# Kernel tuning notes

Measured on AMD Instinct MI355X. Metric: run time of the kernel, lower is better.

The kernel has to match this reference:

```python
import jax, jax.numpy as jnp
import numpy as np

T, N, D_OBS = 32, 32, 64
HID, HEADS, MEM, N_ACT = 512, 4, 128, 16
SECTIONS = [HEADS * HID, HEADS, HID, 1, HID, HID, HEADS, 1, 1, 3 * HEADS]
XI = sum(SECTIONS)


def setup_inputs() -> dict:
    key = jax.random.key(0)
    ks = jax.random.split(key, 8)
    s = 0.02
    return {
        "inputs": jax.random.normal(ks[0], (T, N, D_OBS), jnp.float32),
        "w_ih": jax.random.normal(ks[1], (3 * HID, D_OBS), jnp.float32) * s,
        "w_hh": jax.random.normal(ks[2], (3 * HID, HID), jnp.float32) * s,
        "b_ih": jnp.zeros((3 * HID,), jnp.float32),
        "b_hh": jnp.zeros((3 * HID,), jnp.float32),
        "Wf": jax.random.normal(ks[3], (XI, HID), jnp.float32) * s,
        "bf": jnp.zeros((XI,), jnp.float32),
        "Wa": jax.random.normal(ks[4], (N_ACT, HID), jnp.float32) * s,
        "ba": jnp.zeros((N_ACT,), jnp.float32),
        "Wc": jax.random.normal(ks[5], (1, HID), jnp.float32) * s,
        "bc": jnp.zeros((1,), jnp.float32),
    }


def reference(inputs, w_ih, w_hh, b_ih, b_hh, Wf, bf, Wa, ba, Wc, bc):
    idx = np.cumsum(SECTIONS)[:-1]
    eps = 1e-8

    def step(carry, x_t):
        h, wr, u, ww, M, p, L = carry
        # --- GRU cell (torch convention) ---
        gi = x_t @ w_ih.T + b_ih
        gh = h @ w_hh.T + b_hh
        ir, iz, inn = jnp.split(gi, 3, axis=-1)
        hr, hz, hn = jnp.split(gh, 3, axis=-1)
        rg = jax.nn.sigmoid(ir + hr)
        zg = jax.nn.sigmoid(iz + hz)
        ng = jnp.tanh(inn + rg * hn)
        h = (1 - zg) * ng + zg * h
        # --- interface vector xi ---
        xi = jax.nn.relu(h) @ Wf.T + bf
        Kr, Br, kw, bw, e, v, F_hat, ga, gw, Pi = jnp.split(xi, idx, axis=-1)
        Kr = Kr.reshape(N, HEADS, HID)
        Br = jax.nn.softplus(Br)                      # [N,H]
        bw = jax.nn.softplus(bw)                      # [N,1]
        e = jax.nn.sigmoid(e)                         # [N,HID] erase
        v_w = v                                       # [N,HID] write vec
        F_hat = jax.nn.sigmoid(F_hat)                 # [N,H] free gates
        ga = jax.nn.sigmoid(ga)                       # [N,1]
        gw = jax.nn.sigmoid(gw)                       # [N,1]
        Pi = jax.nn.softmax(Pi.reshape(N, HEADS, 3), axis=-1)
        # --- memory retention & usage ---
        psi = jnp.prod(1 - F_hat[..., None] * wr, axis=1)          # [N,MEM]
        u = (u + ww - u * ww) * psi
        # --- allocation weighting via usage sort ---
        phi = jnp.argsort(u, axis=-1)
        u_sorted = jnp.take_along_axis(u, phi, axis=-1)
        excl = jnp.concatenate(
            [jnp.ones((N, 1), u.dtype), jnp.cumprod(u_sorted[:, :-1], axis=-1)], axis=-1)
        a_sorted = (1 - u_sorted) * excl
        alloc = jnp.zeros_like(u).at[jnp.arange(N)[:, None], phi].set(a_sorted)
        # --- content-based write weighting ---
        Mn = jnp.sqrt(jnp.sum(M * M, axis=-1))                     # [N,MEM]
        kwn = jnp.sqrt(jnp.sum(kw * kw, axis=-1, keepdims=True))   # [N,1]
        cos_w = jnp.einsum('nmd,nd->nm', M, kw) / (Mn * kwn + eps)
        cw = jax.nn.softmax(bw * cos_w, axis=-1)
        ww = gw * (ga * alloc + (1 - ga) * cw)                     # [N,MEM]
        # --- memory write (erase + add outer products) ---
        M = M * (1 - ww[..., None] * e[:, None, :]) + ww[..., None] * v_w[:, None, :]
        # --- precedence & temporal link matrix ---
        p = (1 - jnp.sum(ww, axis=-1, keepdims=True)) * p + ww
        L = (1 - ww[..., None] - ww[:, None, :]) * L + ww[..., None] * p[:, None, :]
        # --- forward/backward read weights ---
        fwd_w = jnp.einsum('nij,nhj->nhi', L, wr)
        bwd_w = jnp.einsum('nji,nhj->nhi', L, wr)
        # --- content-based read weighting ---
        Mn2 = jnp.sqrt(jnp.sum(M * M, axis=-1))                    # [N,MEM]
        Krn = jnp.sqrt(jnp.sum(Kr * Kr, axis=-1, keepdims=True))   # [N,H,1]
        cos_r = jnp.einsum('nmd,nhd->nhm', M, Kr) / (Mn2[:, None, :] * Krn + eps)
        cr = jax.nn.softmax(Br[..., None] * cos_r, axis=-1)
        wr = Pi[..., 0:1] * bwd_w + Pi[..., 1:2] * cr + Pi[..., 2:3] * fwd_w
        # --- read vectors, actor, critic ---
        r_read = jnp.einsum('nmd,nhm->nd', M, wr)                  # sum over heads -> [N,HID]
        a_probs = jax.nn.softmax(r_read @ Wa.T + ba, axis=-1)      # [N,N_ACT]
        val = h @ Wc.T + bc                                        # [N,1]
        return (h, wr, u, ww, M, p, L), jnp.concatenate([a_probs, val], axis=-1)

    z = jnp.zeros
    carry0 = (z((N, HID)), z((N, HEADS, MEM)), z((N, MEM)), z((N, MEM)),
              z((N, MEM, HID)), z((N, MEM)), z((N, MEM, MEM)))
    _, outs = jax.lax.scan(step, carry0, inputs)
    return outs  # [T, N, N_ACT+1]
```

## Files before the change

### kernel.cpp

```cpp
#include <hip/hip_runtime.h>
#include <math.h>

#define TT 32
#define NB 32
#define DOBS 64
#define HID 512
#define HEADS 4
#define MEM 128
#define NACT 16
#define XID 3607
#define G3 1536

__device__ __forceinline__ float sigm(float x){ return 1.0f/(1.0f+__expf(-x)); }
__device__ __forceinline__ float splus(float x){ return fmaxf(x,0.f) + log1pf(__expf(-fabsf(x))); }

__device__ __forceinline__ float wsum64(float s){
    s += __shfl_xor(s,1); s += __shfl_xor(s,2); s += __shfl_xor(s,4);
    s += __shfl_xor(s,8); s += __shfl_xor(s,16);
    float t = s;
    asm volatile("v_permlane32_swap_b32 %0, %1" : "+v"(s), "+v"(t));
    return s + t;
}
__device__ __forceinline__ float rsum_hi(float v){
    float t = v;
    asm volatile("v_permlane16_swap_b32 %0, %1" : "+v"(v), "+v"(t));
    v += t;
    float t2 = v;
    asm volatile("v_permlane32_swap_b32 %0, %1" : "+v"(v), "+v"(t2));
    return v + t2;
}

__global__ __launch_bounds__(256) void k_transpose(const float* __restrict__ src,
                                                   float* __restrict__ dst, int R, int C)
{
    __shared__ float tile[32][33];
    int r0 = blockIdx.x*32, c0 = blockIdx.y*32;
    int tx = threadIdx.x, ty = threadIdx.y;
    #pragma unroll
    for (int yy = 0; yy < 32; yy += 8) {
        int r = r0 + ty + yy, c = c0 + tx;
        if (r < R && c < C) tile[ty+yy][tx] = src[(size_t)r*C + c];
    }
    __syncthreads();
    #pragma unroll
    for (int yy = 0; yy < 32; yy += 8) {
        int c = c0 + ty + yy, r = r0 + tx;
        if (r < R && c < C) dst[(size_t)c*R + r] = tile[tx][ty+yy];
    }
}

__global__ __launch_bounds__(384) void k_gru(
    const float* __restrict__ x,
    const float* __restrict__ wihT,
    const float* __restrict__ whhT,
    const float* __restrict__ b_ih,
    const float* __restrict__ b_hh,
    float* __restrict__ h_all,
    float* hG,
    int* flags)
{
    const int n   = blockIdx.x & 31;
    const int s   = blockIdx.x >> 5;
    const int tid = threadIdx.x;
    const int kq  = tid / 96;
    const int c   = tid % 96;
    const int g   = c >> 5;
    const int r0  = g*512 + s*128 + (c & 31)*4;

    __shared__ float hS[512];
    __shared__ float xS[64];
    __shared__ float4 pI[4][96];
    __shared__ float4 pH[4][96];
    __shared__ float grS[128], gzS[128], giN[128], ghN[128];

    for (int i = tid; i < 512; i += 384) hS[i] = 0.f;

    for (int t = 0; t < TT; ++t) {
        if (tid < 64) xS[tid] = x[((size_t)t*NB + n)*DOBS + tid];
        __syncthreads();
        {
            float4 aI = make_float4(0.f,0.f,0.f,0.f);
            float4 aH = make_float4(0.f,0.f,0.f,0.f);
            const int kx0 = kq*16;
            #pragma unroll 4
            for (int k = kx0; k < kx0+16; ++k) {
                float xv = xS[k];
                float4 w = *(const float4*)(wihT + (size_t)k*G3 + r0);
                aI.x += w.x*xv; aI.y += w.y*xv; aI.z += w.z*xv; aI.w += w.w*xv;
            }
            const int kh0 = kq*128;
            #pragma unroll 4
            for (int k = kh0; k < kh0+128; ++k) {
                float hv = hS[k];
                float4 w = *(const float4*)(whhT + (size_t)k*G3 + r0);
                aH.x += w.x*hv; aH.y += w.y*hv; aH.z += w.z*hv; aH.w += w.w*hv;
            }
            pI[kq][c] = aI; pH[kq][c] = aH;
        }
        __syncthreads();
        {
            const int g2 = tid >> 7, d = tid & 127;
            const int c2 = g2*32 + (d>>2), e = d & 3;
            float AI = 0.f, AH = 0.f;
            #pragma unroll
            for (int q = 0; q < 4; ++q) {
                float4 vi = pI[q][c2], vh = pH[q][c2];
                AI += (e==0)?vi.x:(e==1)?vi.y:(e==2)?vi.z:vi.w;
                AH += (e==0)?vh.x:(e==1)?vh.y:(e==2)?vh.z:vh.w;
            }
            const int rg = g2*512 + s*128 + d;
            AI += b_ih[rg]; AH += b_hh[rg];
            if (g2 == 0)      grS[d] = AI + AH;
            else if (g2 == 1) gzS[d] = AI + AH;
            else              { giN[d] = AI; ghN[d] = AH; }
        }
        __syncthreads();
        if (tid < 128) {
            const int D = s*128 + tid;
            float rg = sigm(grS[tid]);
            float zg = sigm(gzS[tid]);
            float ng = tanhf(giN[tid] + rg*ghN[tid]);
            float hn = (1.f-zg)*ng + zg*hS[D];
            h_all[((size_t)t*NB + n)*HID + D] = hn;
            __hip_atomic_store(&hG[n*HID + D], hn, __ATOMIC_RELAXED, __HIP_MEMORY_SCOPE_AGENT);
        }
        __syncthreads();
        if (t+1 < TT) {
            if (tid == 0) {
                __hip_atomic_fetch_add(&flags[n], 1, __ATOMIC_RELEASE, __HIP_MEMORY_SCOPE_AGENT);
                while (__hip_atomic_load(&flags[n], __ATOMIC_ACQUIRE, __HIP_MEMORY_SCOPE_AGENT) < 4*(t+1)) {
                    __builtin_amdgcn_s_sleep(4);
                }
            }
            __syncthreads();
            for (int i = tid; i < 512; i += 384)
                hS[i] = __hip_atomic_load(&hG[n*HID + i], __ATOMIC_RELAXED, __HIP_MEMORY_SCOPE_AGENT);
        }
    }
}

__global__ __launch_bounds__(256) void k_xi(
    const float* __restrict__ h_all,
    const float* __restrict__ Wf,
    const float* __restrict__ bf,
    float* __restrict__ xi_all)
{
    __shared__ float As[16][132];
    __shared__ float Bs[16][68];
    const int jt = blockIdx.x * 64;
    const int it = blockIdx.y * 128;
    const int tid = threadIdx.x;
    const int lc = tid & 15, lr = tid >> 4;
    const int tx = tid & 15, ty = tid >> 4;
    float acc[8][4] = {};

    for (int k0 = 0; k0 < HID; k0 += 16) {
        #pragma unroll
        for (int s = 0; s < 8; ++s) {
            int i = lr*8 + s;
            As[lc][i] = fmaxf(h_all[(size_t)(it + i)*HID + k0 + lc], 0.f);
        }
        #pragma unroll
        for (int s = 0; s < 4; ++s) {
            int j = lr*4 + s;
            Bs[lc][j] = (jt + j < XID) ? Wf[(size_t)(jt + j)*HID + k0 + lc] : 0.f;
        }
        __syncthreads();
        #pragma unroll
        for (int k = 0; k < 16; ++k) {
            float4 a0 = *(const float4*)&As[k][ty*8];
            float4 a1 = *(const float4*)&As[k][ty*8+4];
            float4 bv = *(const float4*)&Bs[k][tx*4];
            float a[8] = {a0.x,a0.y,a0.z,a0.w,a1.x,a1.y,a1.z,a1.w};
            float b[4] = {bv.x,bv.y,bv.z,bv.w};
            #pragma unroll
            for (int u = 0; u < 8; ++u)
                #pragma unroll
                for (int v = 0; v < 4; ++v) acc[u][v] += a[u]*b[v];
        }
        __syncthreads();
    }
    #pragma unroll
    for (int u = 0; u < 8; ++u)
        #pragma unroll
        for (int v = 0; v < 4; ++v) {
            int i = it + ty*8 + u, j = jt + tx*4 + v;
            if (j < XID) xi_all[(size_t)i*XID + j] = acc[u][v] + bf[j];
        }
}

__global__ __launch_bounds__(64) void k_val(
    const float* __restrict__ h_all, const float* __restrict__ Wc,
    const float* __restrict__ bc, float* __restrict__ out)
{
    const int row = blockIdx.x;
    const int lane = threadIdx.x;
    float acc = 0.f;
    for (int d = lane; d < HID; d += 64) acc += h_all[(size_t)row*HID + d]*Wc[d];
    for (int off = 32; off; off >>= 1) acc += __shfl_down(acc, off);
    if (lane == 0) out[(size_t)row*17 + 16] = acc + bc[0];
}

#define LPAD 132
#define SROW2 576
#define DYN_FLOATS (128*LPAD + 16*SROW2)
#define CIDX(d) ((((d)>>6)*68) + ((d)&63))
#define CIDX2(d) ((((d)>>5)*36) + ((d)&31))

__global__ __launch_bounds__(1024) void k_mem(
    const float* __restrict__ xi_all,
    const float* __restrict__ Wa,
    const float* __restrict__ ba,
    float* __restrict__ out)
{
    extern __shared__ __align__(16) float dynS[];
    float* Lm  = dynS;
    float* scr = dynS + 128*LPAD;

    const int n = blockIdx.x;
    const int tid = threadIdx.x;
    const int lane = tid & 63;
    const int wv = tid >> 6;
    const int m8 = tid >> 3;
    const int q8 = tid & 7;
    const int rp = tid >> 4;
    const int ch = tid & 15;
    const int r0 = rp*2, r1 = r0+1;

    __shared__ __align__(16) float KrC[4*576];
    __shared__ __align__(16) float kwC[576], eC[576], vC[576];
    __shared__ __align__(16) float wrC[4*136];
    __shared__ __align__(16) float r_S[512];
    __shared__ float dotK_S[4][132], fwd_S[4][132], bwd_S[4][132];
    __shared__ float u_S[128], ww_S[128], p_S[128], aS_S[128];
    __shared__ float Mn2_S[128], dw_S[128];
    __shared__ float wred[16][6];
    __shared__ float scal_S[8];
    __shared__ float PiRaw[12];
    __shared__ float Pi_S[4][3], Br_S[4], KrN_S[4], F_S[4];
    __shared__ float ba_S[16], logit_S[16];

    float4 Mreg[16];
    #pragma unroll
    for (int i = 0; i < 16; ++i) Mreg[i] = make_float4(0.f,0.f,0.f,0.f);

    for (int i = tid; i < 128*LPAD; i += 1024) Lm[i] = 0.f;
    if (tid < 16) ba_S[tid] = ba[tid];
    if (tid < 128) { u_S[tid]=0.f; ww_S[tid]=0.f; p_S[tid]=0.f; Mn2_S[tid]=0.f; }
    if (tid < 512) wrC[(tid>>7)*136 + CIDX(tid&127)] = 0.f;

    float waR[8];
    #pragma unroll
    for (int j = 0; j < 8; ++j) waR[j] = Wa[(wv<<9) + lane + (j<<6)];

    const bool hasEx = (tid >= 1000 && tid < 1023);
    int exIdx = 0;
    if (tid >= 1000 && tid < 1004)      exIdx = 2048 + (tid - 1000);
    else if (tid == 1004)               exIdx = 2564;
    else if (tid >= 1005 && tid < 1023) exIdx = 3589 + (tid - 1005);

    const float* xi0 = xi_all + (size_t)n*XID;
    float pKrA = xi0[tid];
    float pKrB = xi0[1024 + tid];
    float pkw = 0.f, pv = 0.f, pe = 0.f;
    if (tid < 512) { pkw = xi0[2052 + tid]; pv = xi0[3077 + tid]; }
    else           { pe  = xi0[2565 + (tid - 512)]; }
    float pex = hasEx ? xi0[exIdx] : 0.f;
    __syncthreads();

    for (int t = 0; t < TT; ++t) {
        float ev2 = 0.f, evA = 0.f;

        {
            int d = tid & 511, hh = tid >> 9;
            int co = CIDX2(d);
            KrC[hh*576 + co]     = pKrA;
            KrC[(2+hh)*576 + co] = pKrB;
        }
        if (tid < 512) { int co = CIDX2(tid); kwC[co] = pkw; vC[co] = pv; }
        else { int s2 = tid - 512; eC[CIDX2(s2)] = sigm(pe); }
        if (hasEx) {
            if (tid < 1004)      Br_S[tid-1000] = splus(pex);
            else if (tid==1004)  scal_S[0] = splus(pex);
            else if (tid < 1009) F_S[tid-1005] = sigm(pex);
            else if (tid==1009)  scal_S[1] = sigm(pex);
            else if (tid==1010)  scal_S[2] = sigm(pex);
            else                 PiRaw[tid-1011] = pex;
        }
        {
            float sA = wsum64(pKrA*pKrA);
            float sB = wsum64(pKrB*pKrB);
            float sK = wsum64(pkw*pkw);
            if (lane == 0) { wred[wv][0]=sA; wred[wv][1]=sB; wred[wv][2]=sK; }
        }
        {
            int tn = (t+1 < TT) ? (t+1) : t;
            const float* xin = xi_all + (size_t)(tn*NB + n)*XID;
            pKrA = xin[tid]; pKrB = xin[1024 + tid];
            if (tid < 512) { pkw = xin[2052 + tid]; pv = xin[3077 + tid]; }
            else           { pe  = xin[2565 + (tid - 512)]; }
            if (hasEx) pex = xin[exIdx];
        }
        __syncthreads();

        if (tid < 4) {
            float s = 0.f;
            #pragma unroll
            for (int w = 0; w < 8; ++w) s += wred[(tid&1)*8 + w][tid>>1];
            KrN_S[tid] = sqrtf(s);
        } else if (tid == 4) {
            float s = 0.f;
            #pragma unroll
            for (int w = 0; w < 8; ++w) s += wred[w][2];
            scal_S[3] = sqrtf(s);
        }
        if (tid < 128) {
            int co = CIDX(tid);
            float psi = (1.f - F_S[0]*wrC[co])      * (1.f - F_S[1]*wrC[136+co])
                      * (1.f - F_S[2]*wrC[272+co])  * (1.f - F_S[3]*wrC[408+co]);
            float uu = u_S[tid], w = ww_S[tid];
            u_S[tid] = (uu + w - uu*w)*psi;
        }
        {
            const float* kwp = kwC + ch*36;
            float dw0 = 0.f, dw1 = 0.f;
            #pragma unroll
            for (int c = 0; c < 8; ++c) {
                float4 kk = *(const float4*)(kwp + 4*c);
                float4 x0 = Mreg[c], x1 = Mreg[8+c];
                dw0 += x0.x*kk.x + x0.y*kk.y + x0.z*kk.z + x0.w*kk.w;
                dw1 += x1.x*kk.x + x1.y*kk.y + x1.z*kk.z + x1.w*kk.w;
            }
            dw0 += __shfl_xor(dw0,1); dw0 += __shfl_xor(dw0,2); dw0 += __shfl_xor(dw0,4); dw0 += __shfl_xor(dw0,8);
            dw1 += __shfl_xor(dw1,1); dw1 += __shfl_xor(dw1,2); dw1 += __shfl_xor(dw1,4); dw1 += __shfl_xor(dw1,8);
            if (ch == 0) { dw_S[r0] = dw0; dw_S[r1] = dw1; }
        }
        __syncthreads();

        {
            float um = u_S[m8];
            float pr = 1.f;
            #pragma unroll
            for (int jj = 0; jj < 16; ++jj) {
                int j = jj*8 + q8;
                float uj = u_S[j];
                pr *= ((uj < um) || (uj == um && j < m8)) ? uj : 1.f;
            }
            pr *= __shfl_xor(pr, 1);
            pr *= __shfl_xor(pr, 2);
            pr *= __shfl_xor(pr, 4);
            if (q8 == 0) aS_S[m8] = (1.f - um)*pr;
        }
        if (tid < 128) {
            float cwv = scal_S[0]*dw_S[tid]/(Mn2_S[tid]*scal_S[3] + 1e-8f);
            evA = __expf(cwv);
            float s = wsum64(evA);
            if (lane == 0) wred[wv][1] = s;
        } else if (tid >= 136 && tid < 140) {
            int h = tid - 136;
            float p0 = PiRaw[3*h], p1 = PiRaw[3*h+1], p2 = PiRaw[3*h+2];
            float mx = fmaxf(p0, fmaxf(p1, p2));
            float e0=__expf(p0-mx), e1=__expf(p1-mx), e2=__expf(p2-mx);
            float s = e0+e1+e2;
            Pi_S[h][0]=e0/s; Pi_S[h][1]=e1/s; Pi_S[h][2]=e2/s;
        }
        __syncthreads();

        if (tid < 128) {
            float cwsum = wred[0][1] + wred[1][1];
            float alloc = aS_S[tid];
            float ga = scal_S[1], gw = scal_S[2];
            float w = gw*(ga*alloc + (1.f-ga)*evA/cwsum);
            ww_S[tid] = w;
            float s = wsum64(w);
            if (lane == 0) wred[wv][0] = s;
        }
        __syncthreads();

        if (tid < 128) {
            float sww = wred[0][0] + wred[1][0];
            p_S[tid] = (1.f - sww)*p_S[tid] + ww_S[tid];
        }
        {
            const int base = ch*36;
            const float* ep  = eC + base;
            const float* vp  = vC + base;
            const float* k0p = KrC + base;
            const float* k1p = KrC + 576 + base;
            const float* k2p = KrC + 1152 + base;
            const float* k3p = KrC + 1728 + base;
            const float ww0 = ww_S[r0], ww1 = ww_S[r1];
            float nrm0=0.f, nrm1=0.f;
            float a0=0.f,a1=0.f,a2=0.f,a3=0.f;
            float b0=0.f,b1=0.f,b2=0.f,b3=0.f;
            #pragma unroll
            for (int c = 0; c < 8; ++c) {
                float4 ee = *(const float4*)(ep + 4*c);
                float4 vv = *(const float4*)(vp + 4*c);
                float4 x  = Mreg[c];
                x.x = x.x*(1.f - ww0*ee.x) + ww0*vv.x;
                x.y = x.y*(1.f - ww0*ee.y) + ww0*vv.y;
                x.z = x.z*(1.f - ww0*ee.z) + ww0*vv.z;
                x.w = x.w*(1.f - ww0*ee.w) + ww0*vv.w;
                Mreg[c] = x;
                nrm0 += x.x*x.x + x.y*x.y + x.z*x.z + x.w*x.w;
                float4 y  = Mreg[8+c];
                y.x = y.x*(1.f - ww1*ee.x) + ww1*vv.x;
                y.y = y.y*(1.f - ww1*ee.y) + ww1*vv.y;
                y.z = y.z*(1.f - ww1*ee.z) + ww1*vv.z;
                y.w = y.w*(1.f - ww1*ee.w) + ww1*vv.w;
                Mreg[8+c] = y;
                nrm1 += y.x*y.x + y.y*y.y + y.z*y.z + y.w*y.w;
                float4 k0 = *(const float4*)(k0p + 4*c);
                float4 k1 = *(const float4*)(k1p + 4*c);
                float4 k2 = *(const float4*)(k2p + 4*c);
                float4 k3 = *(const float4*)(k3p + 4*c);
                a0 += x.x*k0.x + x.y*k0.y + x.z*k0.z + x.w*k0.w;
                a1 += x.x*k1.x + x.y*k1.y + x.z*k1.z + x.w*k1.w;
                a2 += x.x*k2.x + x.y*k2.y + x.z*k2.z + x.w*k2.w;
                a3 += x.x*k3.x + x.y*k3.y + x.z*k3.z + x.w*k3.w;
                b0 += y.x*k0.x + y.y*k0.y + y.z*k0.z + y.w*k0.w;
                b1 += y.x*k1.x + y.y*k1.y + y.z*k1.z + y.w*k1.w;
                b2 += y.x*k2.x + y.y*k2.y + y.z*k2.z + y.w*k2.w;
                b3 += y.x*k3.x + y.y*k3.y + y.z*k3.z + y.w*k3.w;
            }
            #pragma unroll
            for (int mk = 1; mk < 16; mk <<= 1) {
                nrm0 += __shfl_xor(nrm0,mk); nrm1 += __shfl_xor(nrm1,mk);
                a0 += __shfl_xor(a0,mk); a1 += __shfl_xor(a1,mk);
                a2 += __shfl_xor(a2,mk); a3 += __shfl_xor(a3,mk);
                b0 += __shfl_xor(b0,mk); b1 += __shfl_xor(b1,mk);
                b2 += __shfl_xor(b2,mk); b3 += __shfl_xor(b3,mk);
            }
            if (ch < 4) {
                float dA = (ch==0)?a0:(ch==1)?a1:(ch==2)?a2:a3;
                float dB = (ch==0)?b0:(ch==1)?b1:(ch==2)?b2:b3;
                dotK_S[ch][r0] = dA;
                dotK_S[ch][r1] = dB;
            } else if (ch == 4) {
                Mn2_S[r0] = sqrtf(nrm0);
                Mn2_S[r1] = sqrtf(nrm1);
            }
        }
        __syncthreads();

        {
            const int j2 = tid & 127, w8 = tid >> 7;
            float wwj = ww_S[j2], pj = p_S[j2];
            float b0=0.f,b1=0.f,b2=0.f,b3=0.f;
            #pragma unroll
            for (int c2 = 0; c2 < 4; ++c2) {
                const int rr0 = (w8<<4) + (c2<<2);
                const int bidx = CIDX(rr0);
                float4 wwv = *(const float4*)&ww_S[rr0];
                float4 w0v = *(const float4*)&wrC[bidx];
                float4 w1v = *(const float4*)&wrC[136+bidx];
                float4 w2v = *(const float4*)&wrC[272+bidx];
                float4 w3v = *(const float4*)&wrC[408+bidx];
                #pragma unroll
                for (int s4 = 0; s4 < 4; ++s4) {
                    int i2 = rr0 + s4;
                    float wwi = (s4==0)?wwv.x:(s4==1)?wwv.y:(s4==2)?wwv.z:wwv.w;
                    float lold = Lm[i2*LPAD + j2];
                    float ln = (1.f - wwi - wwj)*lold + wwi*pj;
                    Lm[i2*LPAD + j2] = ln;
                    b0 += ln*((s4==0)?w0v.x:(s4==1)?w0v.y:(s4==2)?w0v.z:w0v.w);
                    b1 += ln*((s4==0)?w1v.x:(s4==1)?w1v.y:(s4==2)?w1v.z:w1v.w);
                    b2 += ln*((s4==0)?w2v.x:(s4==1)?w2v.y:(s4==2)?w2v.z:w2v.w);
                    b3 += ln*((s4==0)?w3v.x:(s4==1)?w3v.y:(s4==2)?w3v.z:w3v.w);
                }
            }
            float* sp = scr + w8*SROW2 + j2;
            sp[0]=b0; sp[132]=b1; sp[264]=b2; sp[396]=b3;
        }
        __syncthreads();

        if (tid < 512) {
            int h = tid>>7, mm = tid&127;
            float s = 0.f;
            #pragma unroll
            for (int g = 0; g < 8; ++g) s += scr[g*SROW2 + h*132 + mm];
            bwd_S[h][mm] = s;
        }
        {
            const float* Lr = Lm + m8*LPAD + q8*16;
            const int wb = ((q8>>2)*68) + ((q8&3)<<4);
            float f0=0.f,f1=0.f,f2=0.f,f3=0.f;
            #pragma unroll
            for (int c = 0; c < 4; ++c) {
                float4 lv = *(const float4*)(Lr + 4*c);
                float4 w0 = *(const float4*)&wrC[wb + 4*c];
                float4 w1 = *(const float4*)&wrC[136 + wb + 4*c];
                float4 w2 = *(const float4*)&wrC[272 + wb + 4*c];
                float4 w3 = *(const float4*)&wrC[408 + wb + 4*c];
                f0 += lv.x*w0.x + lv.y*w0.y + lv.z*w0.z + lv.w*w0.w;
                f1 += lv.x*w1.x + lv.y*w1.y + lv.z*w1.z + lv.w*w1.w;
                f2 += lv.x*w2.x + lv.y*w2.y + lv.z*w2.z + lv.w*w2.w;
                f3 += lv.x*w3.x + lv.y*w3.y + lv.z*w3.z + lv.w*w3.w;
            }
            f0 += __shfl_xor(f0,1); f0 += __shfl_xor(f0,2); f0 += __shfl_xor(f0,4);
            f1 += __shfl_xor(f1,1); f1 += __shfl_xor(f1,2); f1 += __shfl_xor(f1,4);
            f2 += __shfl_xor(f2,1); f2 += __shfl_xor(f2,2); f2 += __shfl_xor(f2,4);
            f3 += __shfl_xor(f3,1); f3 += __shfl_xor(f3,2); f3 += __shfl_xor(f3,4);
            if (q8 < 4) fwd_S[q8][m8] = (q8==0) ? f0 : ((q8==1) ? f1 : ((q8==2) ? f2 : f3));
        }
        if (tid < 512) {
            int h = tid>>7, mm = tid&127;
            float scv = Br_S[h]*dotK_S[h][mm]/(Mn2_S[mm]*KrN_S[h] + 1e-8f);
            ev2 = __expf(scv);
            float s = wsum64(ev2);
            if (lane == 0) wred[wv][1] = s;
        }
        __syncthreads();

        if (tid < 512) {
            int h = tid>>7, mm = tid&127;
            float hsum = wred[2*h][1] + wred[2*h+1][1];
            float cr = ev2/hsum;
            wrC[h*136 + CIDX(mm)] = Pi_S[h][0]*bwd_S[h][mm] + Pi_S[h][1]*cr + Pi_S[h][2]*fwd_S[h][mm];
        }
        __syncthreads();

        {
            const int co0 = CIDX(r0), co1 = CIDX(r1);
            float s0 = wrC[co0] + wrC[136+co0] + wrC[272+co0] + wrC[408+co0];
            float s1 = wrC[co1] + wrC[136+co1] + wrC[272+co1] + wrC[408+co1];
            float* sp = scr + wv*SROW2 + ch*36;
            #pragma unroll
            for (int c = 0; c < 8; ++c) {
                float4 x = Mreg[c], y = Mreg[8+c];
                float px = rsum_hi(s0*x.x + s1*y.x);
                float py = rsum_hi(s0*x.y + s1*y.y);
                float pz = rsum_hi(s0*x.z + s1*y.z);
                float pw = rsum_hi(s0*x.w + s1*y.w);
                if (lane < 16) *(float4*)(sp + 4*c) = make_float4(px,py,pz,pw);
            }
        }
        __syncthreads();

        if (tid < 128) {
            const int off = CIDX2(tid<<2);
            float4 r = make_float4(0.f,0.f,0.f,0.f);
            #pragma unroll
            for (int w = 0; w < 16; ++w) {
                float4 v = *(const float4*)&scr[w*SROW2 + off];
                r.x += v.x; r.y += v.y; r.z += v.z; r.w += v.w;
            }
            *(float4*)&r_S[tid<<2] = r;
        }
        __syncthreads();

        {
            float acc = 0.f;
            #pragma unroll
            for (int j = 0; j < 8; ++j) acc += waR[j]*r_S[lane + (j<<6)];
            acc = wsum64(acc);
            if (lane == 0) logit_S[wv] = acc + ba_S[wv];
        }
        __syncthreads();

        if (tid < 16) {
            float lg = logit_S[tid];
            float mx = lg;
            mx = fmaxf(mx, __shfl_xor(mx,1)); mx = fmaxf(mx, __shfl_xor(mx,2));
            mx = fmaxf(mx, __shfl_xor(mx,4)); mx = fmaxf(mx, __shfl_xor(mx,8));
            float ex2 = __expf(lg - mx);
            float s = ex2;
            s += __shfl_xor(s,1); s += __shfl_xor(s,2);
            s += __shfl_xor(s,4); s += __shfl_xor(s,8);
            out[(size_t)(t*NB + n)*17 + tid] = ex2/s;
        }
    }
}

extern "C" void kernel_launch(void* const* d_in, const int* in_sizes, int n_in,
                              void* d_out, int out_size, void* d_ws, size_t ws_size,
                              hipStream_t stream) {
    const float* inp  = (const float*)d_in[0];
    const float* w_ih = (const float*)d_in[1];
    const float* w_hh = (const float*)d_in[2];
    const float* b_ih = (const float*)d_in[3];
    const float* b_hh = (const float*)d_in[4];
    const float* Wf   = (const float*)d_in[5];
    const float* bf   = (const float*)d_in[6];
    const float* Wa   = (const float*)d_in[7];
    const float* ba   = (const float*)d_in[8];
    const float* Wc   = (const float*)d_in[9];
    const float* bc   = (const float*)d_in[10];
    float* out = (float*)d_out;

    float* ws = (float*)d_ws;
    float* wihT   = ws;
    float* whhT   = ws + 98304;
    float* h_all  = ws + 884736;
    float* xi_all = ws + 1409024;
    float* hG     = ws + 5102592;
    int*   flags  = (int*)(ws + 5119008);

    static int dynset = 0;
    if (!dynset) {
        hipFuncSetAttribute(reinterpret_cast<const void*>(k_mem),
                            hipFuncAttributeMaxDynamicSharedMemorySize,
                            DYN_FLOATS*4);
        dynset = 1;
    }

    hipMemsetAsync(flags, 0, NB*sizeof(int), stream);

    dim3 tb(32, 8);
    k_transpose<<<dim3(48, 2),  tb, 0, stream>>>(w_ih, wihT, G3, DOBS);
    k_transpose<<<dim3(48, 16), tb, 0, stream>>>(w_hh, whhT, G3, HID);
    k_gru<<<NB*4, 384, 0, stream>>>(inp, wihT, whhT, b_ih, b_hh, h_all, hG, flags);
    k_xi<<<dim3(57, 8), 256, 0, stream>>>(h_all, Wf, bf, xi_all);
    k_val<<<TT*NB, 64, 0, stream>>>(h_all, Wc, bc, out);
    k_mem<<<NB, 1024, DYN_FLOATS*4, stream>>>(xi_all, Wa, ba, out);
}
```

Measured before the change: 1.176 ms.

## Fuse GRU, xi GEMM and memory kernels into one pipelined persistent launch

Merges the GRU recurrence, the interface-vector GEMM and the per-batch memory kernel into a single launch whose blocks take different roles. Global atomic counters let xi GEMM tiles start once four timesteps of hidden states exist, and let memory blocks start on a time chunk as soon as its xi rows are written. The aim is to overlap the three serial stages instead of running them back to back. It depends on all 240 blocks of 1024 threads being co-resident to avoid deadlock, and the GRU blocks now run 1024-thread blocks with only 384 threads doing work.

```diff
diff --git a/kernel.cpp b/kernel.cpp
--- a/kernel.cpp
+++ b/kernel.cpp
@@ -10,6 +10,9 @@
 #define NACT 16
 #define XID 3607
 #define G3 1536
+
+#define NXIJ 10
+#define NXII 8
 
 __device__ __forceinline__ float sigm(float x){ return 1.0f/(1.0f+__expf(-x)); }
 __device__ __forceinline__ float splus(float x){ return fmaxf(x,0.f) + log1pf(__expf(-fabsf(x))); }
@@ -49,146 +52,6 @@
     }
 }
 
-__global__ __launch_bounds__(384) void k_gru(
-    const float* __restrict__ x,
-    const float* __restrict__ wihT,
-    const float* __restrict__ whhT,
-    const float* __restrict__ b_ih,
-    const float* __restrict__ b_hh,
-    float* __restrict__ h_all,
-    float* hG,
-    int* flags)
-{
-    const int n   = blockIdx.x & 31;
-    const int s   = blockIdx.x >> 5;
-    const int tid = threadIdx.x;
-    const int kq  = tid / 96;
-    const int c   = tid % 96;
-    const int g   = c >> 5;
-    const int r0  = g*512 + s*128 + (c & 31)*4;
-
-    __shared__ float hS[512];
-    __shared__ float xS[64];
-    __shared__ float4 pI[4][96];
-    __shared__ float4 pH[4][96];
-    __shared__ float grS[128], gzS[128], giN[128], ghN[128];
-
-    for (int i = tid; i < 512; i += 384) hS[i] = 0.f;
-
-    for (int t = 0; t < TT; ++t) {
-        if (tid < 64) xS[tid] = x[((size_t)t*NB + n)*DOBS + tid];
-        __syncthreads();
-        {
-            float4 aI = make_float4(0.f,0.f,0.f,0.f);
-            float4 aH = make_float4(0.f,0.f,0.f,0.f);
-            const int kx0 = kq*16;
-            #pragma unroll 4
-            for (int k = kx0; k < kx0+16; ++k) {
-                float xv = xS[k];
-                float4 w = *(const float4*)(wihT + (size_t)k*G3 + r0);
-                aI.x += w.x*xv; aI.y += w.y*xv; aI.z += w.z*xv; aI.w += w.w*xv;
-            }
-            const int kh0 = kq*128;
-            #pragma unroll 4
-            for (int k = kh0; k < kh0+128; ++k) {
-                float hv = hS[k];
-                float4 w = *(const float4*)(whhT + (size_t)k*G3 + r0);
-                aH.x += w.x*hv; aH.y += w.y*hv; aH.z += w.z*hv; aH.w += w.w*hv;
-            }
-            pI[kq][c] = aI; pH[kq][c] = aH;
-        }
-        __syncthreads();
-        {
-            const int g2 = tid >> 7, d = tid & 127;
-            const int c2 = g2*32 + (d>>2), e = d & 3;
-            float AI = 0.f, AH = 0.f;
-            #pragma unroll
-            for (int q = 0; q < 4; ++q) {
-                float4 vi = pI[q][c2], vh = pH[q][c2];
-                AI += (e==0)?vi.x:(e==1)?vi.y:(e==2)?vi.z:vi.w;
-                AH += (e==0)?vh.x:(e==1)?vh.y:(e==2)?vh.z:vh.w;
-            }
-            const int rg = g2*512 + s*128 + d;
-            AI += b_ih[rg]; AH += b_hh[rg];
-            if (g2 == 0)      grS[d] = AI + AH;
-            else if (g2 == 1) gzS[d] = AI + AH;
-            else              { giN[d] = AI; ghN[d] = AH; }
-        }
-        __syncthreads();
-        if (tid < 128) {
-            const int D = s*128 + tid;
-            float rg = sigm(grS[tid]);
-            float zg = sigm(gzS[tid]);
-            float ng = tanhf(giN[tid] + rg*ghN[tid]);
-            float hn = (1.f-zg)*ng + zg*hS[D];
-            h_all[((size_t)t*NB + n)*HID + D] = hn;
-            __hip_atomic_store(&hG[n*HID + D], hn, __ATOMIC_RELAXED, __HIP_MEMORY_SCOPE_AGENT);
-        }
-        __syncthreads();
-        if (t+1 < TT) {
-            if (tid == 0) {
-                __hip_atomic_fetch_add(&flags[n], 1, __ATOMIC_RELEASE, __HIP_MEMORY_SCOPE_AGENT);
-                while (__hip_atomic_load(&flags[n], __ATOMIC_ACQUIRE, __HIP_MEMORY_SCOPE_AGENT) < 4*(t+1)) {
-                    __builtin_amdgcn_s_sleep(4);
-                }
-            }
-            __syncthreads();
-            for (int i = tid; i < 512; i += 384)
-                hS[i] = __hip_atomic_load(&hG[n*HID + i], __ATOMIC_RELAXED, __HIP_MEMORY_SCOPE_AGENT);
-        }
-    }
-}
-
-__global__ __launch_bounds__(256) void k_xi(
-    const float* __restrict__ h_all,
-    const float* __restrict__ Wf,
-    const float* __restrict__ bf,
-    float* __restrict__ xi_all)
-{
-    __shared__ float As[16][132];
-    __shared__ float Bs[16][68];
-    const int jt = blockIdx.x * 64;
-    const int it = blockIdx.y * 128;
-    const int tid = threadIdx.x;
-    const int lc = tid & 15, lr = tid >> 4;
-    const int tx = tid & 15, ty = tid >> 4;
-    float acc[8][4] = {};
-
-    for (int k0 = 0; k0 < HID; k0 += 16) {
-        #pragma unroll
-        for (int s = 0; s < 8; ++s) {
-            int i = lr*8 + s;
-            As[lc][i] = fmaxf(h_all[(size_t)(it + i)*HID + k0 + lc], 0.f);
-        }
-        #pragma unroll
-        for (int s = 0; s < 4; ++s) {
-            int j = lr*4 + s;
-            Bs[lc][j] = (jt + j < XID) ? Wf[(size_t)(jt + j)*HID + k0 + lc] : 0.f;
-        }
-        __syncthreads();
-        #pragma unroll
-        for (int k = 0; k < 16; ++k) {
-            float4 a0 = *(const float4*)&As[k][ty*8];
-            float4 a1 = *(const float4*)&As[k][ty*8+4];
-            float4 bv = *(const float4*)&Bs[k][tx*4];
-            float a[8] = {a0.x,a0.y,a0.z,a0.w,a1.x,a1.y,a1.z,a1.w};
-            float b[4] = {bv.x,bv.y,bv.z,bv.w};
-            #pragma unroll
-            for (int u = 0; u < 8; ++u)
-                #pragma unroll
-                for (int v = 0; v < 4; ++v) acc[u][v] += a[u]*b[v];
-        }
-        __syncthreads();
-    }
-    #pragma unroll
-    for (int u = 0; u < 8; ++u)
-        #pragma unroll
-        for (int v = 0; v < 4; ++v) {
-            int i = it + ty*8 + u, j = jt + tx*4 + v;
-            if (j < XID) xi_all[(size_t)i*XID + j] = acc[u][v] + bf[j];
-        }
-}
-
 __global__ __launch_bounds__(64) void k_val(
     const float* __restrict__ h_all, const float* __restrict__ Wc,
     const float* __restrict__ bc, float* __restrict__ out)
@@ -207,18 +70,182 @@
 #define CIDX(d) ((((d)>>6)*68) + ((d)&63))
 #define CIDX2(d) ((((d)>>5)*36) + ((d)&31))
 
-__global__ __launch_bounds__(1024) void k_mem(
-    const float* __restrict__ xi_all,
+__global__ __launch_bounds__(1024) void k_fused(
+    const float* __restrict__ x,
+    const float* __restrict__ wihT,
+    const float* __restrict__ whhT,
+    const float* __restrict__ b_ih,
+    const float* __restrict__ b_hh,
+    float* h_all,
+    const float* __restrict__ Wf,
+    const float* __restrict__ bf,
+    float* xi_all,
     const float* __restrict__ Wa,
     const float* __restrict__ ba,
-    float* __restrict__ out)
+    float* __restrict__ out,
+    float* hG,
+    int* flagsN,
+    int* gstep,
+    int* xidone)
 {
     extern __shared__ __align__(16) float dynS[];
+    const int bid = blockIdx.x;
+    const int tid = threadIdx.x;
+
+    if (bid >= 32 && bid < 160) {
+        const int g = bid - 32;
+        const int n = g & 31, sl = g >> 5;
+        float* hS = dynS;
+        float* xS = dynS + 512;
+        float* pI = dynS + 576;
+        float* pH = dynS + 2112;
+        float* grS = dynS + 3648;
+        float* gzS = dynS + 3776;
+        float* giN = dynS + 3904;
+        float* ghN = dynS + 4032;
+
+        const int kq = tid / 96;
+        const int c  = tid % 96;
+        const int gg = c >> 5;
+        const int r0 = gg*512 + sl*128 + (c & 31)*4;
+
+        for (int i = tid; i < 512; i += 1024) hS[i] = 0.f;
+
+        for (int t = 0; t < TT; ++t) {
+            if (tid < 64) xS[tid] = x[((size_t)t*NB + n)*DOBS + tid];
+            __syncthreads();
+            if (tid < 384) {
+                float4 aI = make_float4(0.f,0.f,0.f,0.f);
+                float4 aH = make_float4(0.f,0.f,0.f,0.f);
+                const int kx0 = kq*16;
+                #pragma unroll 4
+                for (int k = kx0; k < kx0+16; ++k) {
+                    float xv = xS[k];
+                    float4 w = *(const float4*)(wihT + (size_t)k*G3 + r0);
+                    aI.x += w.x*xv; aI.y += w.y*xv; aI.z += w.z*xv; aI.w += w.w*xv;
+                }
+                const int kh0 = kq*128;
+                #pragma unroll 4
+                for (int k = kh0; k < kh0+128; ++k) {
+                    float hv = hS[k];
+                    float4 w = *(const float4*)(whhT + (size_t)k*G3 + r0);
+                    aH.x += w.x*hv; aH.y += w.y*hv; aH.z += w.z*hv; aH.w += w.w*hv;
+                }
+                *(float4*)&pI[(kq*96 + c)*4] = aI;
+                *(float4*)&pH[(kq*96 + c)*4] = aH;
+            }
+            __syncthreads();
+            if (tid < 384) {
+                const int g2 = tid >> 7, d = tid & 127;
+                const int c2 = g2*32 + (d>>2), e = d & 3;
+                float AI = 0.f, AH = 0.f;
+                #pragma unroll
+                for (int q = 0; q < 4; ++q) {
+                    AI += pI[(q*96 + c2)*4 + e];
+                    AH += pH[(q*96 + c2)*4 + e];
+                }
+                const int rg = g2*512 + sl*128 + d;
+                AI += b_ih[rg]; AH += b_hh[rg];
+                if (g2 == 0)      grS[d] = AI + AH;
+                else if (g2 == 1) gzS[d] = AI + AH;
+                else              { giN[d] = AI; ghN[d] = AH; }
+            }
+            __syncthreads();
+            if (tid < 128) {
+                const int D = sl*128 + tid;
+                float rg = sigm(grS[tid]);
+                float zg = sigm(gzS[tid]);
+                float ng = tanhf(giN[tid] + rg*ghN[tid]);
+                float hn = (1.f-zg)*ng + zg*hS[D];
+                h_all[((size_t)t*NB + n)*HID + D] = hn;
+                __hip_atomic_store(&hG[n*HID + D], hn, __ATOMIC_RELAXED, __HIP_MEMORY_SCOPE_AGENT);
+            }
+            __syncthreads();
+            if (tid == 0) {
+                __hip_atomic_fetch_add(gstep, 1, __ATOMIC_RELEASE, __HIP_MEMORY_SCOPE_AGENT);
+                if (t+1 < TT) {
+                    __hip_atomic_fetch_add(&flagsN[n], 1, __ATOMIC_RELEASE, __HIP_MEMORY_SCOPE_AGENT);
+                    while (__hip_atomic_load(&flagsN[n], __ATOMIC_ACQUIRE, __HIP_MEMORY_SCOPE_AGENT) < 4*(t+1)) {
+                        __builtin_amdgcn_s_sleep(4);
+                    }
+                }
+            }
+            if (t+1 < TT) {
+                __syncthreads();
+                for (int i = tid; i < 512; i += 1024)
+                    hS[i] = __hip_atomic_load(&hG[n*HID + i], __ATOMIC_RELAXED, __HIP_MEMORY_SCOPE_AGENT);
+            }
+        }
+        return;
+    }
+
+    if (bid >= 160) {
+        const int q2 = bid - 160;
+        const int jtile = q2 % NXIJ, itile = q2 / NXIJ;
+        const int it = itile*128, jt = jtile*384;
+        float* As = dynS;
+        float* Bs = dynS + 16*132;
+        const int q  = tid >> 8;
+        const int t8 = tid & 255;
+        const int lc = t8 & 15, lr = t8 >> 4;
+        const int tx = t8 & 15, ty = t8 >> 4;
+        const int i2 = tid >> 4;
+
+        if (tid == 0) {
+            while (__hip_atomic_load(gstep, __ATOMIC_RELAXED, __HIP_MEMORY_SCOPE_AGENT) < 128*(4*itile+4)) {
+                __builtin_amdgcn_s_sleep(8);
+            }
+        }
+        __syncthreads();
+        __builtin_amdgcn_fence(__ATOMIC_ACQUIRE, "agent");
+
+        float acc[8][6] = {};
+        for (int k0 = 0; k0 < HID; k0 += 16) {
+            #pragma unroll
+            for (int s = 0; s < 2; ++s) {
+                int i = i2*2 + s;
+                float hv = h_all[(size_t)(it + i)*HID + k0 + lc];
+                As[lc*132 + i] = fmaxf(hv, 0.f);
+            }
+            #pragma unroll
+            for (int s = 0; s < 6; ++s) {
+                int j = lr*6 + s;
+                int col = jt + q*96 + j;
+                Bs[lc*400 + q*100 + j] = (col < XID) ? Wf[(size_t)col*HID + k0 + lc] : 0.f;
+            }
+            __syncthreads();
+            #pragma unroll
+            for (int k = 0; k < 16; ++k) {
+                float a[8], b[6];
+                #pragma unroll
+                for (int u = 0; u < 8; ++u) a[u] = As[k*132 + ty*8 + u];
+                #pragma unroll
+                for (int v = 0; v < 6; ++v) b[v] = Bs[k*400 + q*100 + tx*6 + v];
+                #pragma unroll
+                for (int u = 0; u < 8; ++u)
+                    #pragma unroll
+                    for (int v = 0; v < 6; ++v) acc[u][v] += a[u]*b[v];
+            }
+            __syncthreads();
+        }
+        #pragma unroll
+        for (int u = 0; u < 8; ++u)
+            #pragma unroll
+            for (int v = 0; v < 6; ++v) {
+                int i = it + ty*8 + u, j = jt + q*96 + tx*6 + v;
+                if (j < XID) xi_all[(size_t)i*XID + j] = acc[u][v] + bf[j];
+            }
+        __syncthreads();
+        if (tid == 0)
+            __hip_atomic_fetch_add(&xidone[itile], 1, __ATOMIC_RELEASE, __HIP_MEMORY_SCOPE_AGENT);
+        return;
+    }
+
+    {
     float* Lm  = dynS;
     float* scr = dynS + 128*LPAD;
 
-    const int n = blockIdx.x;
-    const int tid = threadIdx.x;
+    const int n = bid;
     const int lane = tid & 63;
     const int wv = tid >> 6;
     const int m8 = tid >> 3;
@@ -259,6 +286,14 @@
     else if (tid == 1004)               exIdx = 2564;
     else if (tid >= 1005 && tid < 1023) exIdx = 3589 + (tid - 1005);
 
+    if (tid == 0) {
+        while (__hip_atomic_load(&xidone[0], __ATOMIC_RELAXED, __HIP_MEMORY_SCOPE_AGENT) < NXIJ) {
+            __builtin_amdgcn_s_sleep(8);
+        }
+    }
+    __syncthreads();
+    __builtin_amdgcn_fence(__ATOMIC_ACQUIRE, "agent");
+
     const float* xi0 = xi_all + (size_t)n*XID;
     float pKrA = xi0[tid];
     float pKrB = xi0[1024 + tid];
@@ -266,7 +301,6 @@
     if (tid < 512) { pkw = xi0[2052 + tid]; pv = xi0[3077 + tid]; }
     else           { pe  = xi0[2565 + (tid - 512)]; }
     float pex = hasEx ? xi0[exIdx] : 0.f;
-    __syncthreads();
 
     for (int t = 0; t < TT; ++t) {
         float ev2 = 0.f, evA = 0.f;
@@ -295,6 +329,15 @@
         }
         {
             int tn = (t+1 < TT) ? (t+1) : t;
+            if (t+1 < TT && ((t+1) & 3) == 0) {
+                if (tid == 0) {
+                    while (__hip_atomic_load(&xidone[(t+1)>>2], __ATOMIC_RELAXED, __HIP_MEMORY_SCOPE_AGENT) < NXIJ) {
+                        __builtin_amdgcn_s_sleep(8);
+                    }
+                }
+                __syncthreads();
+                __builtin_amdgcn_fence(__ATOMIC_ACQUIRE, "agent");
+            }
             const float* xin = xi_all + (size_t)(tn*NB + n)*XID;
             pKrA = xin[tid]; pKrB = xin[1024 + tid];
             if (tid < 512) { pkw = xin[2052 + tid]; pv = xin[3077 + tid]; }
@@ -397,32 +440,32 @@
             for (int c = 0; c < 8; ++c) {
                 float4 ee = *(const float4*)(ep + 4*c);
                 float4 vv = *(const float4*)(vp + 4*c);
-                float4 x  = Mreg[c];
-                x.x = x.x*(1.f - ww0*ee.x) + ww0*vv.x;
-                x.y = x.y*(1.f - ww0*ee.y) + ww0*vv.y;
-                x.z = x.z*(1.f - ww0*ee.z) + ww0*vv.z;
-                x.w = x.w*(1.f - ww0*ee.w) + ww0*vv.w;
-                Mreg[c] = x;
-                nrm0 += x.x*x.x + x.y*x.y + x.z*x.z + x.w*x.w;
-                float4 y  = Mreg[8+c];
-                y.x = y.x*(1.f - ww1*ee.x) + ww1*vv.x;
-                y.y = y.y*(1.f - ww1*ee.y) + ww1*vv.y;
-                y.z = y.z*(1.f - ww1*ee.z) + ww1*vv.z;
-                y.w = y.w*(1.f - ww1*ee.w) + ww1*vv.w;
-                Mreg[8+c] = y;
-                nrm1 += y.x*y.x + y.y*y.y + y.z*y.z + y.w*y.w;
+                float4 xx  = Mreg[c];
+                xx.x = xx.x*(1.f - ww0*ee.x) + ww0*vv.x;
+                xx.y = xx.y*(1.f - ww0*ee.y) + ww0*vv.y;
+                xx.z = xx.z*(1.f - ww0*ee.z) + ww0*vv.z;
+                xx.w = xx.w*(1.f - ww0*ee.w) + ww0*vv.w;
+                Mreg[c] = xx;
+                nrm0 += xx.x*xx.x + xx.y*xx.y + xx.z*xx.z + xx.w*xx.w;
+                float4 yy  = Mreg[8+c];
+                yy.x = yy.x*(1.f - ww1*ee.x) + ww1*vv.x;
+                yy.y = yy.y*(1.f - ww1*ee.y) + ww1*vv.y;
+                yy.z = yy.z*(1.f - ww1*ee.z) + ww1*vv.z;
+                yy.w = yy.w*(1.f - ww1*ee.w) + ww1*vv.w;
+                Mreg[8+c] = yy;
+                nrm1 += yy.x*yy.x + yy.y*yy.y + yy.z*yy.z + yy.w*yy.w;
                 float4 k0 = *(const float4*)(k0p + 4*c);
                 float4 k1 = *(const float4*)(k1p + 4*c);
                 float4 k2 = *(const float4*)(k2p + 4*c);
                 float4 k3 = *(const float4*)(k3p + 4*c);
-                a0 += x.x*k0.x + x.y*k0.y + x.z*k0.z + x.w*k0.w;
-                a1 += x.x*k1.x + x.y*k1.y + x.z*k1.z + x.w*k1.w;
-                a2 += x.x*k2.x + x.y*k2.y + x.z*k2.z + x.w*k2.w;
-                a3 += x.x*k3.x + x.y*k3.y + x.z*k3.z + x.w*k3.w;
-                b0 += y.x*k0.x + y.y*k0.y + y.z*k0.z + y.w*k0.w;
-                b1 += y.x*k1.x + y.y*k1.y + y.z*k1.z + y.w*k1.w;
-                b2 += y.x*k2.x + y.y*k2.y + y.z*k2.z + y.w*k2.w;
-                b3 += y.x*k3.x + y.y*k3.y + y.z*k3.z + y.w*k3.w;
+                a0 += xx.x*k0.x + xx.y*k0.y + xx.z*k0.z + xx.w*k0.w;
+                a1 += xx.x*k1.x + xx.y*k1.y + xx.z*k1.z + xx.w*k1.w;
+                a2 += xx.x*k2.x + xx.y*k2.y + xx.z*k2.z + xx.w*k2.w;
+                a3 += xx.x*k3.x + xx.y*k3.y + xx.z*k3.z + xx.w*k3.w;
+                b0 += yy.x*k0.x + yy.y*k0.y + yy.z*k0.z + yy.w*k0.w;
+                b1 += yy.x*k1.x + yy.y*k1.y + yy.z*k1.z + yy.w*k1.w;
+                b2 += yy.x*k2.x + yy.y*k2.y + yy.z*k2.z + yy.w*k2.w;
+                b3 += yy.x*k3.x + yy.y*k3.y + yy.z*k3.z + yy.w*k3.w;
             }
             #pragma unroll
             for (int mk = 1; mk < 16; mk <<= 1) {
@@ -528,11 +571,11 @@
             float* sp = scr + wv*SROW2 + ch*36;
             #pragma unroll
             for (int c = 0; c < 8; ++c) {
-                float4 x = Mreg[c], y = Mreg[8+c];
-                float px = rsum_hi(s0*x.x + s1*y.x);
-                float py = rsum_hi(s0*x.y + s1*y.y);
-                float pz = rsum_hi(s0*x.z + s1*y.z);
-                float pw = rsum_hi(s0*x.w + s1*y.w);
+                float4 xx = Mreg[c], yy = Mreg[8+c];
+                float px = rsum_hi(s0*xx.x + s1*yy.x);
+                float py = rsum_hi(s0*xx.y + s1*yy.y);
+                float pz = rsum_hi(s0*xx.z + s1*yy.z);
+                float pw = rsum_hi(s0*xx.w + s1*yy.w);
                 if (lane < 16) *(float4*)(sp + 4*c) = make_float4(px,py,pz,pw);
             }
         }
@@ -570,6 +613,7 @@
             s += __shfl_xor(s,4); s += __shfl_xor(s,8);
             out[(size_t)(t*NB + n)*17 + tid] = ex2/s;
         }
+    }
     }
 }
 
@@ -595,23 +639,25 @@
     float* h_all  = ws + 884736;
     float* xi_all = ws + 1409024;
     float* hG     = ws + 5102592;
-    int*   flags  = (int*)(ws + 5119008);
+    int*   flagsN = (int*)(ws + 5119008);
+    int*   gstep  = flagsN + 32;
+    int*   xidone = gstep + 1;
 
     static int dynset = 0;
     if (!dynset) {
-        hipFuncSetAttribute(reinterpret_cast<const void*>(k_mem),
+        hipFuncSetAttribute(reinterpret_cast<const void*>(k_fused),
                             hipFuncAttributeMaxDynamicSharedMemorySize,
                             DYN_FLOATS*4);
         dynset = 1;
     }
 
-    hipMemsetAsync(flags, 0, NB*sizeof(int), stream);
+    hipMemsetAsync(flagsN, 0, 64*sizeof(int), stream);
 
     dim3 tb(32, 8);
     k_transpose<<<dim3(48, 2),  tb, 0, stream>>>(w_ih, wihT, G3, DOBS);
     k_transpose<<<dim3(48, 16), tb, 0, stream>>>(w_hh, whhT, G3, HID);
-    k_gru<<<NB*4, 384, 0, stream>>>(inp, wihT, whhT, b_ih, b_hh, h_all, hG, flags);
-    k_xi<<<dim3(57, 8), 256, 0, stream>>>(h_all, Wf, bf, xi_all);
+    k_fused<<<32 + 128 + NXII*NXIJ, 1024, DYN_FLOATS*4, stream>>>(
+        inp, wihT, whhT, b_ih, b_hh, h_all, Wf, bf, xi_all, Wa, ba, out,
+        hG, flagsN, gstep, xidone);
     k_val<<<TT*NB, 64, 0, stream>>>(h_all, Wc, bc, out);
-    k_mem<<<NB, 1024, DYN_FLOATS*4, stream>>>(xi_all, Wa, ba, out);
 }
```

Result: slower. 1.236 ms (+5.1%).
